# Performance work log

Hardware: AMD Instinct MI355X
Metric: run time of the kernel (lower is better)

## Reference

```python
import jax, jax.numpy as jnp
import numpy as np

SHIFT = 0.0          # drr shift
DENS_OFFSET = 0.3    # density property subtracts 0.3 before regulator


def _affine_inverse(affine, pts):
    # apply inverse of 4x4 affine to [..., 3] points (world -> voxel index space)
    inv = jnp.linalg.inv(affine)
    return pts @ inv[:3, :3].T + inv[:3, 3]


def setup_inputs() -> dict:
    key = jax.random.key(0)
    k1, k2, k3, k4 = jax.random.split(key, 4)
    D = H = W = 256
    B, N = 1, 40000  # 200x200 detector -> one ray per pixel

    _density = 0.1 * jax.random.normal(k1, (D, H, W), dtype=jnp.float32)

    # voxel-index -> world affine: unit spacing, translated origin
    affine = jnp.eye(4, dtype=jnp.float32).at[:3, 3].set(
        jnp.array([-10.0, -10.0, -10.0], dtype=jnp.float32))

    # x-ray point source on one side of the volume (slightly jittered per ray)
    src_center = jnp.array([-60.0, 118.0, 118.0], dtype=jnp.float32)
    source = src_center + 0.5 * jax.random.normal(k2, (B, N, 3), dtype=jnp.float32)

    # detector targets on the far side, spanning the volume in y/z
    ty = jax.random.uniform(k3, (B, N, 1), minval=-10.0, maxval=250.0)
    tz = jax.random.uniform(k4, (B, N, 1), minval=-10.0, maxval=250.0)
    tx = jnp.full((B, N, 1), 320.0, dtype=jnp.float32)
    target = jnp.concatenate([tx, ty, tz], axis=-1).astype(jnp.float32)

    return {"_density": _density, "source": source, "target": target,
            "affine": affine, "n_points": 500}


def reference(_density, source, target, affine, n_points):
    # density regulator: sigmoid(_density - shift - 0.3)
    density = jax.nn.sigmoid(_density - SHIFT - DENS_OFFSET)

    # ray length in world space: [B, 1, N]
    raylength = jnp.linalg.norm(target - source, axis=-1)[:, None, :]

    # map endpoints into voxel index space
    s = _affine_inverse(affine, source)   # [B, N, 3]
    t = _affine_inverse(affine, target)   # [B, N, 3]

    # sample n_points uniformly along each ray: pts [B, N, P, 3]
    alphas = jnp.linspace(0.0, 1.0, n_points, dtype=source.dtype)
    pts = s[..., None, :] + alphas[:, None] * (t - s)[..., None, :]

    # trilinear gather (zero outside volume), samples [B, N, P]
    coords = [pts[..., 0], pts[..., 1], pts[..., 2]]
    samples = jax.scipy.ndimage.map_coordinates(
        density, coords, order=1, mode="constant", cval=0.0)

    # integrate along ray: sum * (raylength / n_points) -> [B, 1, N]
    img = samples.sum(axis=-1)[:, None, :] * raylength / n_points
    return img
```

## Files before the change

kernel.cpp:

```cpp
#include <hip/hip_runtime.h>
#include <hip/hip_fp16.h>

#define NB 64
#define NBUCKETS (NB * NB)

typedef unsigned int uint2v __attribute__((ext_vector_type(2)));

__device__ __forceinline__ float sigm(float v)
{
    return 1.0f / (1.0f + __expf(0.3f - v));
}

__device__ __forceinline__ float2 unpack_h2(unsigned int w)
{
    __half2 h = *reinterpret_cast<__half2*>(&w);
    return make_float2(__low2float(h), __high2float(h));
}

__global__ __launch_bounds__(256) void pack_kernel(
    const float* __restrict__ dens, unsigned int* __restrict__ P)
{
    __shared__ float tile[32][33];
    int bid = blockIdx.x;
    int y0 = (bid & 31) * 8;
    int xt = ((bid >> 5) & 7) * 32;
    int zt = (bid >> 8) * 32;
    int tz = threadIdx.x & 31;
    int tr = threadIdx.x >> 5;

    float prev[4];
    int ytop = y0 + 8;
    if (ytop < 256) {
        #pragma unroll
        for (int i = 0; i < 4; ++i) {
            int xr = tr + 8 * i;
            tile[xr][tz] = sigm(dens[(size_t)(xt + xr) * 65536 +
                                     (size_t)ytop * 256 + (zt + tz)]);
        }
        __syncthreads();
        #pragma unroll
        for (int i = 0; i < 4; ++i)
            prev[i] = tile[tz][tr + 8 * i];
        __syncthreads();
    } else {
        #pragma unroll
        for (int i = 0; i < 4; ++i) prev[i] = 0.0f;
    }

    for (int yy = 7; yy >= 0; --yy) {
        int y = y0 + yy;
        #pragma unroll
        for (int i = 0; i < 4; ++i) {
            int xr = tr + 8 * i;
            tile[xr][tz] = sigm(dens[(size_t)(xt + xr) * 65536 +
                                     (size_t)y * 256 + (zt + tz)]);
        }
        __syncthreads();
        #pragma unroll
        for (int i = 0; i < 4; ++i) {
            int zr = tr + 8 * i;
            float cur = tile[tz][zr];
            __half2 h = __floats2half2_rn(cur, prev[i]);
            P[((zt + zr) << 16) | (y << 8) | (xt + tz)] =
                *reinterpret_cast<unsigned int*>(&h);
            prev[i] = cur;
        }
        __syncthreads();
    }
}

__device__ __forceinline__ int ray_bucket(const float* __restrict__ target, int r)
{
    float ty = target[3 * r + 1];
    float tz = target[3 * r + 2];
    int bu = (int)((ty + 10.0f) * (NB / 260.0f));
    int bv = (int)((tz + 10.0f) * (NB / 260.0f));
    bu = min(max(bu, 0), NB - 1);
    bv = min(max(bv, 0), NB - 1);
    int m = 0;
    #pragma unroll
    for (int b = 0; b < 6; ++b)
        m |= (((bu >> b) & 1) << (2 * b)) | (((bv >> b) & 1) << (2 * b + 1));
    return m;
}

__global__ __launch_bounds__(256) void zero_kernel(int* __restrict__ p, int n)
{
    int i = blockIdx.x * 256 + threadIdx.x;
    if (i < n) p[i] = 0;
}

__global__ __launch_bounds__(256) void hist_kernel(
    const float* __restrict__ target, int* __restrict__ hist, int nrays)
{
    int r = blockIdx.x * 256 + threadIdx.x;
    if (r < nrays) atomicAdd(&hist[ray_bucket(target, r)], 1);
}

__global__ __launch_bounds__(256) void scan_kernel(
    const int* __restrict__ hist, int* __restrict__ offs, int* __restrict__ cursor)
{
    __shared__ int part[256];
    int t = threadIdx.x;
    int v[16];
    int s = 0;
    #pragma unroll
    for (int i = 0; i < 16; ++i) {
        v[i] = hist[t * 16 + i];
        s += v[i];
    }
    part[t] = s;
    __syncthreads();
    for (int d = 1; d < 256; d <<= 1) {
        int add = (t >= d) ? part[t - d] : 0;
        __syncthreads();
        part[t] += add;
        __syncthreads();
    }
    int base = part[t] - s;
    #pragma unroll
    for (int i = 0; i < 16; ++i) {
        offs[t * 16 + i] = base;
        base += v[i];
        cursor[t * 16 + i] = 0;
    }
}

__global__ __launch_bounds__(256) void scatter_kernel(
    const float* __restrict__ target, const int* __restrict__ offs,
    int* __restrict__ cursor, int* __restrict__ perm, int nrays)
{
    int r = blockIdx.x * 256 + threadIdx.x;
    if (r >= nrays) return;
    int bkt = ray_bucket(target, r);
    int pos = offs[bkt] + atomicAdd(&cursor[bkt], 1);
    perm[pos] = r;
}

__device__ __forceinline__ float2 fetchP(
    const unsigned int* __restrict__ P, int x, int y, int z)
{
    if ((unsigned)x < 256u && (unsigned)z < 256u) {
        if ((unsigned)y < 256u)
            return unpack_h2(P[(z << 16) | (y << 8) | x]);
        if (y == -1) {
            float2 v = unpack_h2(P[(z << 16) | x]);
            return make_float2(0.0f, v.x);
        }
    }
    return make_float2(0.0f, 0.0f);
}

__global__ __launch_bounds__(256) void drr_kernel(
    const unsigned int* __restrict__ P,
    const float*  __restrict__ source,
    const float*  __restrict__ target,
    const float*  __restrict__ affine,
    const int*    __restrict__ npts_ptr,
    const int*    __restrict__ perm,
    float*        __restrict__ out,
    int nrays)
{
    const int lane  = threadIdx.x & 63;
    const int sub   = lane >> 4;
    const int phase = lane & 15;
    const int wave  = threadIdx.x >> 6;
    int slot = blockIdx.x * 16 + wave * 4 + sub;
    bool valid = (slot < nrays);
    if (slot >= nrays) slot = nrays - 1;
    const int ray = perm ? perm[slot] : slot;
    const int npts = *npts_ptr;

    float a00 = affine[0], a01 = affine[1], a02 = affine[2],  b0 = affine[3];
    float a10 = affine[4], a11 = affine[5], a12 = affine[6],  b1 = affine[7];
    float a20 = affine[8], a21 = affine[9], a22 = affine[10], b2 = affine[11];
    float det = a00 * (a11 * a22 - a12 * a21)
              - a01 * (a10 * a22 - a12 * a20)
              + a02 * (a10 * a21 - a11 * a20);
    float rdet = 1.0f / det;
    float i00 =  (a11 * a22 - a12 * a21) * rdet;
    float i01 = -(a01 * a22 - a02 * a21) * rdet;
    float i02 =  (a01 * a12 - a02 * a11) * rdet;
    float i10 = -(a10 * a22 - a12 * a20) * rdet;
    float i11 =  (a00 * a22 - a02 * a20) * rdet;
    float i12 = -(a00 * a12 - a02 * a10) * rdet;
    float i20 =  (a10 * a21 - a11 * a20) * rdet;
    float i21 = -(a00 * a21 - a01 * a20) * rdet;
    float i22 =  (a00 * a11 - a01 * a10) * rdet;
    float it0 = -(i00 * b0 + i01 * b1 + i02 * b2);
    float it1 = -(i10 * b0 + i11 * b1 + i12 * b2);
    float it2 = -(i20 * b0 + i21 * b1 + i22 * b2);

    float sx = source[3 * ray + 0], sy = source[3 * ray + 1], sz = source[3 * ray + 2];
    float tx = target[3 * ray + 0], ty = target[3 * ray + 1], tz = target[3 * ray + 2];
    float dwx = tx - sx, dwy = ty - sy, dwz = tz - sz;
    float rl = sqrtf(dwx * dwx + dwy * dwy + dwz * dwz);

    float vsx = i00 * sx + i01 * sy + i02 * sz + it0;
    float vsy = i10 * sx + i11 * sy + i12 * sz + it1;
    float vsz = i20 * sx + i21 * sy + i22 * sz + it2;
    float vtx = i00 * tx + i01 * ty + i02 * tz + it0;
    float vty = i10 * tx + i11 * ty + i12 * tz + it1;
    float vtz = i20 * tx + i21 * ty + i22 * tz + it2;
    float vdx = vtx - vsx, vdy = vty - vsy, vdz = vtz - vsz;

    float lo = 0.0f, hi = 1.0f;
    {
        float s3v[3] = {vsx, vsy, vsz};
        float d3v[3] = {vdx, vdy, vdz};
        #pragma unroll
        for (int k = 0; k < 3; ++k) {
            if (fabsf(d3v[k]) > 1e-8f) {
                float a = (-1.0f - s3v[k]) / d3v[k];
                float b = (256.0f - s3v[k]) / d3v[k];
                lo = fmaxf(lo, fminf(a, b));
                hi = fminf(hi, fmaxf(a, b));
            } else if (s3v[k] <= -1.0f || s3v[k] >= 256.0f) {
                lo = 1.0f; hi = 0.0f;
            }
        }
    }
    const float stepN = (float)(npts > 1 ? npts - 1 : 1);
    int pstart = max(0, (int)floorf(lo * stepN) - 1);
    int pend   = min(npts - 1, (int)ceilf(hi * stepN) + 1);

    const float step = 1.0f / stepN;
    float acc = 0.0f;

    float al0 = (float)(pstart + phase) * step;
    float x = fmaf(al0, vdx, vsx);
    float y = fmaf(al0, vdy, vsy);
    float z = fmaf(al0, vdz, vsz);
    float d16x = 16.0f * step * vdx;
    float d16y = 16.0f * step * vdy;
    float d16z = 16.0f * step * vdz;

    #pragma unroll 4
    for (int p = pstart + phase; p <= pend; p += 16) {
        float fx = floorf(x), fy = floorf(y), fz = floorf(z);
        int ix = (int)fx, iy = (int)fy, iz = (int)fz;
        float wx = x - fx, wy = y - fy, wz = z - fz;
        x += d16x; y += d16y; z += d16z;

        float2 p00, p01, p10, p11;
        bool interior = ((unsigned)ix < 255u) & ((unsigned)iy < 256u) &
                        ((unsigned)iz < 255u);
        if (interior) {
            int idx = (iz << 16) | (iy << 8) | ix;
            uint2v va, vb;
            __builtin_memcpy(&va, P + idx, 8);
            __builtin_memcpy(&vb, P + idx + 65536, 8);
            p00 = unpack_h2(va.x);
            p01 = unpack_h2(va.y);
            p10 = unpack_h2(vb.x);
            p11 = unpack_h2(vb.y);
        } else {
            p00 = fetchP(P, ix,     iy, iz);
            p01 = fetchP(P, ix + 1, iy, iz);
            p10 = fetchP(P, ix,     iy, iz + 1);
            p11 = fetchP(P, ix + 1, iy, iz + 1);
        }
        float c00 = p00.x + wy * (p00.y - p00.x);
        float c10 = p01.x + wy * (p01.y - p01.x);
        float c01 = p10.x + wy * (p10.y - p10.x);
        float c11 = p11.x + wy * (p11.y - p11.x);
        float c0  = c00 + wz * (c01 - c00);
        float c1  = c10 + wz * (c11 - c10);
        acc += c0 + wx * (c1 - c0);
    }

    #pragma unroll
    for (int off = 8; off > 0; off >>= 1)
        acc += __shfl_down(acc, off, 16);

    if (phase == 0 && valid)
        out[ray] = acc * rl / (float)npts;
}

extern "C" void kernel_launch(void* const* d_in, const int* in_sizes, int n_in,
                              void* d_out, int out_size, void* d_ws, size_t ws_size,
                              hipStream_t stream)
{
    const float* dens   = (const float*)d_in[0];
    const float* source = (const float*)d_in[1];
    const float* target = (const float*)d_in[2];
    const float* affine = (const float*)d_in[3];
    const int*   npts   = (const int*)d_in[4];
    float* out = (float*)d_out;

    const int nvox  = in_sizes[0];
    const int nrays = in_sizes[1] / 3;

    size_t packBytes = ((size_t)nvox * 4 + 255) & ~(size_t)255;
    size_t sortBytes = (size_t)(3 * NBUCKETS + nrays) * sizeof(int);

    const int ray_blocks = (nrays + 15) / 16;

    unsigned int* P = (unsigned int*)d_ws;
    int* hist   = (int*)((char*)d_ws + packBytes);
    int* offs   = hist + NBUCKETS;
    int* cursor = offs + NBUCKETS;
    int* perm   = cursor + NBUCKETS;
    const bool srt = (ws_size >= packBytes + sortBytes);
    int* permArg = srt ? perm : nullptr;

    if (srt) {
        zero_kernel<<<(NBUCKETS + 255) / 256, 256, 0, stream>>>(hist, NBUCKETS);
        hist_kernel<<<(nrays + 255) / 256, 256, 0, stream>>>(target, hist, nrays);
        scan_kernel<<<1, 256, 0, stream>>>(hist, offs, cursor);
        scatter_kernel<<<(nrays + 255) / 256, 256, 0, stream>>>(target, offs, cursor, perm, nrays);
    }

    pack_kernel<<<2048, 256, 0, stream>>>(dens, P);
    drr_kernel<<<ray_blocks, 256, 0, stream>>>(
        P, source, target, affine, npts, permArg, out, nrays);
}
```

Before: 172.0 us.

## Quantize density to 8-bit 2x2 corner bricks and fuse ray sort into one kernel

The packed volume changes from fp16 pairs (y,y+1) to 8-bit quantized 2x2 (y,z) corner groups in one 32-bit word. Each trilinear sample then needs a single 8-byte load instead of two, which cuts gather traffic and cache footprint. The four ray-sorting kernels become one single-block kernel using shared-memory histograms, which removes launch overhead. Rays now use 8 lanes each instead of 16. Quantizing to 8 bits adds about 1/510 error per voxel, and the single-block sort runs serially on one CU.

Result: slower. 202.0 us (+17.4%).

```diff
diff --git a/kernel.cpp b/kernel.cpp
--- a/kernel.cpp
+++ b/kernel.cpp
@@ -11,61 +11,56 @@
     return 1.0f / (1.0f + __expf(0.3f - v));
 }
 
-__device__ __forceinline__ float2 unpack_h2(unsigned int w)
-{
-    __half2 h = *reinterpret_cast<__half2*>(&w);
-    return make_float2(__low2float(h), __high2float(h));
-}
-
-__global__ __launch_bounds__(256) void pack_kernel(
-    const float* __restrict__ dens, unsigned int* __restrict__ P)
-{
-    __shared__ float tile[32][33];
+__device__ __forceinline__ unsigned int q8(float s)
+{
+    return (unsigned int)fmaf(s, 255.0f, 0.5f);
+}
+
+__global__ __launch_bounds__(256) void packq4_kernel(
+    const float* __restrict__ dens, unsigned int* __restrict__ Q)
+{
+    __shared__ float S[2][33 * 33 + 1];
     int bid = blockIdx.x;
     int y0 = (bid & 31) * 8;
     int xt = ((bid >> 5) & 7) * 32;
     int zt = (bid >> 8) * 32;
-    int tz = threadIdx.x & 31;
-    int tr = threadIdx.x >> 5;
-
-    float prev[4];
-    int ytop = y0 + 8;
-    if (ytop < 256) {
+    int tid = threadIdx.x;
+
+    auto load_plane = [&](int y) {
+        float* Sp = S[y & 1];
+        #pragma unroll
+        for (int r = 0; r < 5; ++r) {
+            int li = r * 256 + tid;
+            if (li < 33 * 32) {
+                int zc = li % 33, xr = li / 33;
+                int zz = zt + zc;
+                float v = 0.0f;
+                if (zz < 256 && y < 256)
+                    v = sigm(dens[(size_t)(xt + xr) * 65536 +
+                                  (size_t)y * 256 + zz]);
+                Sp[zc * 33 + xr] = v;
+            }
+        }
+    };
+
+    load_plane(y0 + 8);
+    for (int y = y0 + 7; y >= y0; --y) {
+        __syncthreads();
+        load_plane(y);
+        __syncthreads();
+        const float* S0 = S[y & 1];
+        const float* S1 = S[(y + 1) & 1];
+        int xo = tid & 31;
+        int zb = tid >> 5;
         #pragma unroll
         for (int i = 0; i < 4; ++i) {
-            int xr = tr + 8 * i;
-            tile[xr][tz] = sigm(dens[(size_t)(xt + xr) * 65536 +
-                                     (size_t)ytop * 256 + (zt + tz)]);
-        }
-        __syncthreads();
-        #pragma unroll
-        for (int i = 0; i < 4; ++i)
-            prev[i] = tile[tz][tr + 8 * i];
-        __syncthreads();
-    } else {
-        #pragma unroll
-        for (int i = 0; i < 4; ++i) prev[i] = 0.0f;
-    }
-
-    for (int yy = 7; yy >= 0; --yy) {
-        int y = y0 + yy;
-        #pragma unroll
-        for (int i = 0; i < 4; ++i) {
-            int xr = tr + 8 * i;
-            tile[xr][tz] = sigm(dens[(size_t)(xt + xr) * 65536 +
-                                     (size_t)y * 256 + (zt + tz)]);
-        }
-        __syncthreads();
-        #pragma unroll
-        for (int i = 0; i < 4; ++i) {
-            int zr = tr + 8 * i;
-            float cur = tile[tz][zr];
-            __half2 h = __floats2half2_rn(cur, prev[i]);
-            P[((zt + zr) << 16) | (y << 8) | (xt + tz)] =
-                *reinterpret_cast<unsigned int*>(&h);
-            prev[i] = cur;
-        }
-        __syncthreads();
+            int zo = zb + 8 * i;
+            unsigned int q = q8(S0[zo * 33 + xo])
+                           | (q8(S1[zo * 33 + xo]) << 8)
+                           | (q8(S0[(zo + 1) * 33 + xo]) << 16)
+                           | (q8(S1[(zo + 1) * 33 + xo]) << 24);
+            Q[((zt + zo) << 16) | (y << 8) | (xt + xo)] = q;
+        }
     }
 }
 
@@ -84,34 +79,27 @@
     return m;
 }
 
-__global__ __launch_bounds__(256) void zero_kernel(int* __restrict__ p, int n)
-{
-    int i = blockIdx.x * 256 + threadIdx.x;
-    if (i < n) p[i] = 0;
-}
-
-__global__ __launch_bounds__(256) void hist_kernel(
-    const float* __restrict__ target, int* __restrict__ hist, int nrays)
-{
-    int r = blockIdx.x * 256 + threadIdx.x;
-    if (r < nrays) atomicAdd(&hist[ray_bucket(target, r)], 1);
-}
-
-__global__ __launch_bounds__(256) void scan_kernel(
-    const int* __restrict__ hist, int* __restrict__ offs, int* __restrict__ cursor)
-{
-    __shared__ int part[256];
+__global__ __launch_bounds__(1024) void sort_kernel(
+    const float* __restrict__ target, int* __restrict__ perm, int nrays)
+{
+    __shared__ int hist[NBUCKETS];
+    __shared__ int offs[NBUCKETS];
+    __shared__ int part[1024];
     int t = threadIdx.x;
-    int v[16];
+
+    for (int i = t; i < NBUCKETS; i += 1024) hist[i] = 0;
+    __syncthreads();
+    for (int r = t; r < nrays; r += 1024)
+        atomicAdd(&hist[ray_bucket(target, r)], 1);
+    __syncthreads();
+
+    int v[4];
     int s = 0;
     #pragma unroll
-    for (int i = 0; i < 16; ++i) {
-        v[i] = hist[t * 16 + i];
-        s += v[i];
-    }
+    for (int i = 0; i < 4; ++i) { v[i] = hist[t * 4 + i]; s += v[i]; }
     part[t] = s;
     __syncthreads();
-    for (int d = 1; d < 256; d <<= 1) {
+    for (int d = 1; d < 1024; d <<= 1) {
         int add = (t >= d) ? part[t - d] : 0;
         __syncthreads();
         part[t] += add;
@@ -119,40 +107,49 @@
     }
     int base = part[t] - s;
     #pragma unroll
-    for (int i = 0; i < 16; ++i) {
-        offs[t * 16 + i] = base;
-        base += v[i];
-        cursor[t * 16 + i] = 0;
-    }
-}
-
-__global__ __launch_bounds__(256) void scatter_kernel(
-    const float* __restrict__ target, const int* __restrict__ offs,
-    int* __restrict__ cursor, int* __restrict__ perm, int nrays)
-{
-    int r = blockIdx.x * 256 + threadIdx.x;
-    if (r >= nrays) return;
-    int bkt = ray_bucket(target, r);
-    int pos = offs[bkt] + atomicAdd(&cursor[bkt], 1);
-    perm[pos] = r;
-}
-
-__device__ __forceinline__ float2 fetchP(
-    const unsigned int* __restrict__ P, int x, int y, int z)
-{
-    if ((unsigned)x < 256u && (unsigned)z < 256u) {
-        if ((unsigned)y < 256u)
-            return unpack_h2(P[(z << 16) | (y << 8) | x]);
-        if (y == -1) {
-            float2 v = unpack_h2(P[(z << 16) | x]);
-            return make_float2(0.0f, v.x);
-        }
-    }
-    return make_float2(0.0f, 0.0f);
+    for (int i = 0; i < 4; ++i) { offs[t * 4 + i] = base; base += v[i]; }
+    __syncthreads();
+
+    for (int i = t; i < NBUCKETS; i += 1024) hist[i] = 0;
+    __syncthreads();
+    for (int r = t; r < nrays; r += 1024) {
+        int b = ray_bucket(target, r);
+        int pos = offs[b] + atomicAdd(&hist[b], 1);
+        perm[pos] = r;
+    }
+}
+
+__device__ __forceinline__ float4 fetchB(
+    const unsigned int* __restrict__ Q, int x, int y, int z)
+{
+    if ((unsigned)x < 256u) {
+        bool yin = (unsigned)y < 256u;
+        bool zin = (unsigned)z < 256u;
+        if (yin && zin) {
+            unsigned int v = Q[(z << 16) | (y << 8) | x];
+            return make_float4((float)(v & 255u), (float)((v >> 8) & 255u),
+                               (float)((v >> 16) & 255u), (float)(v >> 24));
+        }
+        if (y == -1 && zin) {
+            unsigned int v = Q[(z << 16) | x];
+            return make_float4(0.0f, (float)(v & 255u),
+                               0.0f, (float)((v >> 16) & 255u));
+        }
+        if (yin && z == -1) {
+            unsigned int v = Q[(y << 8) | x];
+            return make_float4(0.0f, 0.0f,
+                               (float)(v & 255u), (float)((v >> 8) & 255u));
+        }
+        if (y == -1 && z == -1) {
+            unsigned int v = Q[x];
+            return make_float4(0.0f, 0.0f, 0.0f, (float)(v & 255u));
+        }
+    }
+    return make_float4(0.0f, 0.0f, 0.0f, 0.0f);
 }
 
 __global__ __launch_bounds__(256) void drr_kernel(
-    const unsigned int* __restrict__ P,
+    const unsigned int* __restrict__ Q,
     const float*  __restrict__ source,
     const float*  __restrict__ target,
     const float*  __restrict__ affine,
@@ -162,10 +159,10 @@
     int nrays)
 {
     const int lane  = threadIdx.x & 63;
-    const int sub   = lane >> 4;
-    const int phase = lane & 15;
+    const int sub   = lane >> 3;
+    const int phase = lane & 7;
     const int wave  = threadIdx.x >> 6;
-    int slot = blockIdx.x * 16 + wave * 4 + sub;
+    int slot = blockIdx.x * 32 + wave * 8 + sub;
     bool valid = (slot < nrays);
     if (slot >= nrays) slot = nrays - 1;
     const int ray = perm ? perm[slot] : slot;
@@ -231,50 +228,48 @@
     float x = fmaf(al0, vdx, vsx);
     float y = fmaf(al0, vdy, vsy);
     float z = fmaf(al0, vdz, vsz);
-    float d16x = 16.0f * step * vdx;
-    float d16y = 16.0f * step * vdy;
-    float d16z = 16.0f * step * vdz;
+    float d8x = 8.0f * step * vdx;
+    float d8y = 8.0f * step * vdy;
+    float d8z = 8.0f * step * vdz;
 
     #pragma unroll 4
-    for (int p = pstart + phase; p <= pend; p += 16) {
+    for (int p = pstart + phase; p <= pend; p += 8) {
         float fx = floorf(x), fy = floorf(y), fz = floorf(z);
         int ix = (int)fx, iy = (int)fy, iz = (int)fz;
         float wx = x - fx, wy = y - fy, wz = z - fz;
-        x += d16x; y += d16y; z += d16z;
-
-        float2 p00, p01, p10, p11;
+        x += d8x; y += d8y; z += d8z;
+
+        float4 A, B;
         bool interior = ((unsigned)ix < 255u) & ((unsigned)iy < 256u) &
-                        ((unsigned)iz < 255u);
+                        ((unsigned)iz < 256u);
         if (interior) {
             int idx = (iz << 16) | (iy << 8) | ix;
-            uint2v va, vb;
-            __builtin_memcpy(&va, P + idx, 8);
-            __builtin_memcpy(&vb, P + idx + 65536, 8);
-            p00 = unpack_h2(va.x);
-            p01 = unpack_h2(va.y);
-            p10 = unpack_h2(vb.x);
-            p11 = unpack_h2(vb.y);
+            uint2v v;
+            __builtin_memcpy(&v, Q + idx, 8);
+            unsigned int va = v.x, vb = v.y;
+            A = make_float4((float)(va & 255u), (float)((va >> 8) & 255u),
+                            (float)((va >> 16) & 255u), (float)(va >> 24));
+            B = make_float4((float)(vb & 255u), (float)((vb >> 8) & 255u),
+                            (float)((vb >> 16) & 255u), (float)(vb >> 24));
         } else {
-            p00 = fetchP(P, ix,     iy, iz);
-            p01 = fetchP(P, ix + 1, iy, iz);
-            p10 = fetchP(P, ix,     iy, iz + 1);
-            p11 = fetchP(P, ix + 1, iy, iz + 1);
-        }
-        float c00 = p00.x + wy * (p00.y - p00.x);
-        float c10 = p01.x + wy * (p01.y - p01.x);
-        float c01 = p10.x + wy * (p10.y - p10.x);
-        float c11 = p11.x + wy * (p11.y - p11.x);
-        float c0  = c00 + wz * (c01 - c00);
-        float c1  = c10 + wz * (c11 - c10);
-        acc += c0 + wx * (c1 - c0);
+            A = fetchB(Q, ix,     iy, iz);
+            B = fetchB(Q, ix + 1, iy, iz);
+        }
+        float ca = fmaf(wy, A.y - A.x, A.x);
+        float cb = fmaf(wy, A.w - A.z, A.z);
+        float e  = fmaf(wz, cb - ca, ca);
+        float cc = fmaf(wy, B.y - B.x, B.x);
+        float cd = fmaf(wy, B.w - B.z, B.z);
+        float f  = fmaf(wz, cd - cc, cc);
+        acc += fmaf(wx, f - e, e);
     }
 
     #pragma unroll
-    for (int off = 8; off > 0; off >>= 1)
-        acc += __shfl_down(acc, off, 16);
+    for (int off = 4; off > 0; off >>= 1)
+        acc += __shfl_down(acc, off, 8);
 
     if (phase == 0 && valid)
-        out[ray] = acc * rl / (float)npts;
+        out[ray] = acc * rl / ((float)npts * 255.0f);
 }
 
 extern "C" void kernel_launch(void* const* d_in, const int* in_sizes, int n_in,
@@ -291,27 +286,19 @@
     const int nvox  = in_sizes[0];
     const int nrays = in_sizes[1] / 3;
 
-    size_t packBytes = ((size_t)nvox * 4 + 255) & ~(size_t)255;
-    size_t sortBytes = (size_t)(3 * NBUCKETS + nrays) * sizeof(int);
-
-    const int ray_blocks = (nrays + 15) / 16;
-
-    unsigned int* P = (unsigned int*)d_ws;
-    int* hist   = (int*)((char*)d_ws + packBytes);
-    int* offs   = hist + NBUCKETS;
-    int* cursor = offs + NBUCKETS;
-    int* perm   = cursor + NBUCKETS;
-    const bool srt = (ws_size >= packBytes + sortBytes);
+    size_t qBytes    = ((size_t)nvox * 4 + 255) & ~(size_t)255;
+    size_t sortBytes = (size_t)nrays * sizeof(int);
+
+    unsigned int* Q = (unsigned int*)d_ws;
+    int* perm = (int*)((char*)d_ws + qBytes);
+    const bool srt = (ws_size >= qBytes + sortBytes);
     int* permArg = srt ? perm : nullptr;
 
-    if (srt) {
-        zero_kernel<<<(NBUCKETS + 255) / 256, 256, 0, stream>>>(hist, NBUCKETS);
-        hist_kernel<<<(nrays + 255) / 256, 256, 0, stream>>>(target, hist, nrays);
-        scan_kernel<<<1, 256, 0, stream>>>(hist, offs, cursor);
-        scatter_kernel<<<(nrays + 255) / 256, 256, 0, stream>>>(target, offs, cursor, perm, nrays);
-    }
-
-    pack_kernel<<<2048, 256, 0, stream>>>(dens, P);
-    drr_kernel<<<ray_blocks, 256, 0, stream>>>(
-        P, source, target, affine, npts, permArg, out, nrays);
-}
+    if (srt)
+        sort_kernel<<<1, 1024, 0, stream>>>(target, perm, nrays);
+
+    packq4_kernel<<<2048, 256, 0, stream>>>(dens, Q);
+
+    drr_kernel<<<(nrays + 31) / 32, 256, 0, stream>>>(
+        Q, source, target, affine, npts, permArg, out, nrays);
+}
```
